# Kernel optimization log

Measured on AMD Instinct MI355X. Metric: run time of the kernel, lower is better.

## Reference

```python
import jax, jax.numpy as jnp
import numpy as np

EMBED_DIM = 32
HIDDEN_DIM = 64
N = 1024
LN_EPS = 1e-5


def setup_inputs() -> dict:
    key = jax.random.key(0)
    ks = jax.random.split(key, 8)
    d, h = EMBED_DIM, HIDDEN_DIM
    s1 = 1.0 / np.sqrt(2 * d)
    s2 = 1.0 / np.sqrt(h)
    return {
        "node_embeddings": jax.random.normal(ks[0], (N, d), dtype=jnp.float32),
        # Linear(2d -> h), stored as (2d, h) for x @ W
        "W1": jax.random.uniform(ks[1], (2 * d, h), jnp.float32, -s1, s1),
        "b1": jnp.zeros((h,), jnp.float32),
        "g1": jnp.ones((h,), jnp.float32),
        "be1": jnp.zeros((h,), jnp.float32),
        "W2": jax.random.uniform(ks[2], (h, h), jnp.float32, -s2, s2),
        "b2": jnp.zeros((h,), jnp.float32),
        "g2": jnp.ones((h,), jnp.float32),
        "be2": jnp.zeros((h,), jnp.float32),
        "W3": jax.random.uniform(ks[3], (h, 1), jnp.float32, -s2, s2),
        "b3": jnp.zeros((1,), jnp.float32),
    }


def _layernorm(x, gamma, beta):
    mu = jnp.mean(x, axis=-1, keepdims=True)
    var = jnp.mean(jnp.square(x - mu), axis=-1, keepdims=True)
    return (x - mu) * jax.lax.rsqrt(var + LN_EPS) * gamma + beta


def reference(node_embeddings, W1, b1, g1, be1, W2, b2, g2, be2, W3, b3):
    n, d = node_embeddings.shape
    # pair_emb = cat([src_emb, dst_emb], -1); first linear applied without
    # materializing the concat: split W1 into src/dst halves.
    W1s, W1d = W1[:d], W1[d:]
    hs = node_embeddings @ W1s          # (N, h)
    hd = node_embeddings @ W1d          # (N, h)
    h = hs[:, None, :] + hd[None, :, :] + b1   # (N, N, h)
    h = jax.nn.relu(_layernorm(h, g1, be1))
    h = jax.nn.relu(_layernorm(h @ W2 + b2, g2, be2))
    out = jax.nn.sigmoid((h @ W3 + b3)[..., 0])  # (N, N)
    return out
```

## Files before the change

kernel.cpp:

```cpp
#include <hip/hip_runtime.h>
#include <hip/hip_bf16.h>

#define NN 1024
#define ED 32
#define HD 64
#define LN_EPS 1e-5f
#define LPAD 68

typedef short bf16x8 __attribute__((ext_vector_type(8)));
typedef float f32x4 __attribute__((ext_vector_type(4)));

#define OFF_HS   0
#define OFF_HDB  65536
#define OFF_G1   131072
#define OFF_BE1  131136
#define OFF_B2   131200
#define OFF_G2   131264
#define OFF_BE2  131328
#define OFF_W3   131392
#define OFF_B3   131456
#define OFF_SB2  131457
#define OFF_W2F  131460

__device__ __forceinline__ bool buf_is_f32(const void* g1) {
  return *(const unsigned int*)g1 == 0x3F800000u;
}
template <bool F32>
__device__ __forceinline__ float ld(const void* p, int i) {
  return F32 ? ((const float*)p)[i]
             : __bfloat162float(((const __hip_bfloat16*)p)[i]);
}
__device__ __forceinline__ unsigned short f2bf(float f) {
  unsigned int b = __builtin_bit_cast(unsigned int, f);
  b += 0x7FFFu + ((b >> 16) & 1u);
  return (unsigned short)(b >> 16);
}
__device__ __forceinline__ unsigned int pack2bf(float a, float b) {
  return (unsigned int)f2bf(a) | ((unsigned int)f2bf(b) << 16);
}
__device__ __forceinline__ f32x4 splat4(float v) { f32x4 r = {v, v, v, v}; return r; }

template <int CTRL>
__device__ __forceinline__ float dpp_add(float v) {
  int m = __builtin_amdgcn_update_dpp(0, __builtin_bit_cast(int, v), CTRL, 0xF, 0xF, true);
  return v + __builtin_bit_cast(float, m);
}
__device__ __forceinline__ float red16(float v) {
  v = dpp_add<0xB1>(v);
  v = dpp_add<0x4E>(v);
  v = dpp_add<0x124>(v);
  v = dpp_add<0x128>(v);
  return v;
}

template <bool F32>
__device__ void prep_body(const void* E, const void* W1, const void* b1,
                          const void* g1, const void* be1, const void* W2,
                          const void* b2, const void* g2, const void* be2,
                          const void* W3, const void* b3, float* ws) {
  const int i = blockIdx.x, t = threadIdx.x;
  if (i < NN) {
    __shared__ float e[ED];
    if (t < ED) e[t] = ld<F32>(E, i * ED + t);
    __syncthreads();
    int k = t & 63;
    int wofs = (t >= 64 ? ED * HD : 0);
    float acc = 0.f;
#pragma unroll
    for (int c = 0; c < ED; ++c)
      acc = fmaf(e[c], ld<F32>(W1, wofs + c * HD + k), acc);
    if (t >= 64) ws[OFF_HDB + i * HD + k] = acc + ld<F32>(b1, k);
    else         ws[OFF_HS  + i * HD + k] = acc;
  } else {
    __shared__ float rs[64];
    if (t < 64) {
      ws[OFF_G1  + t] = ld<F32>(g1,  t);
      ws[OFF_BE1 + t] = ld<F32>(be1, t);
      ws[OFF_B2  + t] = ld<F32>(b2,  t);
      ws[OFF_G2  + t] = ld<F32>(g2,  t);
      ws[OFF_BE2 + t] = ld<F32>(be2, t);
      ws[OFF_W3  + t] = ld<F32>(W3,  t);
      float s = 0.f;
      for (int n = 0; n < HD; ++n) s += ld<F32>(W2, t * HD + n);
      rs[t] = s;
    }
    if (t == 64) {
      float s = 0.f;
      for (int n = 0; n < HD; ++n) s += ld<F32>(b2, n);
      ws[OFF_SB2] = s;
    }
    if (t == 65) ws[OFF_B3] = ld<F32>(b3, 0);
    uint4* d4 = (uint4*)(ws + OFF_W2F);
    for (int base = t * 16; base < 4096; base += 128 * 16) {
      int nt = (base >> 9) & 3, kc = base >> 11;
#pragma unroll
      for (int half = 0; half < 2; ++half) {
        int lv = ((base >> 3) + half) & 63;
        int k0 = kc * 32 + ((lv >> 4) & 3) * 8;
        int n = nt * 16 + (lv & 15);
        unsigned int u4[4];
#pragma unroll
        for (int jj = 0; jj < 4; ++jj)
          u4[jj] = pack2bf(ld<F32>(W2, (k0 + 2 * jj) * HD + n),
                           ld<F32>(W2, (k0 + 2 * jj + 1) * HD + n));
        d4[(base >> 3) + half] = make_uint4(u4[0], u4[1], u4[2], u4[3]);
      }
    }
    __syncthreads();
    unsigned short* st = (unsigned short*)(ws + OFF_W2F) + 4096;
    for (int s = t; s < 1024; s += 128) {
      int j = s & 7, lv = (s >> 3) & 63, kc = s >> 9;
      st[s] = f2bf(rs[kc * 32 + ((lv >> 4) & 3) * 8 + j]);
    }
  }
}

__global__ __launch_bounds__(128) void prep_kern(
    const void* E, const void* W1, const void* b1, const void* g1,
    const void* be1, const void* W2, const void* b2, const void* g2,
    const void* be2, const void* W3, const void* b3, float* ws) {
  if (buf_is_f32(g1))
    prep_body<true >(E, W1, b1, g1, be1, W2, b2, g2, be2, W3, b3, ws);
  else
    prep_body<false>(E, W1, b1, g1, be1, W2, b2, g2, be2, W3, b3, ws);
}

__global__ __launch_bounds__(256, 3) void pair_kern(
    const float* __restrict__ ws, float* __restrict__ out) {
  __shared__ float shsd[2][16 * LPAD];
  __shared__ __align__(16) unsigned int X[256 * 32];
  const int t = threadIdx.x;
  const int bi = blockIdx.y, bj = blockIdx.x;
  const int l = t & 63, w = t >> 6;
  const int q = l >> 4, ln = l & 15;
  const float inv = 1.f / 64.f;

  {
    int r = t >> 4, c4 = t & 15;
    ((float4*)(shsd[0] + r * LPAD))[c4] = ((const float4*)(ws + OFF_HS  + (bi * 16 + r) * HD))[c4];
    ((float4*)(shsd[1] + r * LPAD))[c4] = ((const float4*)(ws + OFF_HDB + (bj * 16 + r) * HD))[c4];
  }
  __syncthreads();

  {
    int il = t >> 4, jl = t & 15;
    const f32x4* av = (const f32x4*)(shsd[0] + il * LPAD);
    const f32x4* bv = (const f32x4*)(shsd[1] + jl * LPAD);
    f32x4 xv[16];
    f32x4 s4 = splat4(0.f), q4 = splat4(0.f);
#pragma unroll
    for (int c = 0; c < 16; ++c) {
      f32x4 x = av[c] + bv[c];
      xv[c] = x;
      s4 += x;
      q4 = __builtin_elementwise_fma(x, x, q4);
    }
    float sum = (s4[0] + s4[1]) + (s4[2] + s4[3]);
    float ssq = (q4[0] + q4[1]) + (q4[2] + q4[3]);
    float mu = sum * inv;
    float r1 = rsqrtf(fmaf(-mu, mu, ssq * inv) + LN_EPS);
    f32x4 r1v = splat4(r1), nm = splat4(-mu * r1), zero = splat4(0.f);
    unsigned int ub[32];
#pragma unroll
    for (int c = 0; c < 16; ++c) {
      f32x4 g, be;
#pragma unroll
      for (int e = 0; e < 4; ++e) {
        g[e]  = ws[OFF_G1  + c * 4 + e];
        be[e] = ws[OFF_BE1 + c * 4 + e];
      }
      f32x4 u = __builtin_elementwise_fma(xv[c], r1v, nm);
      f32x4 v = __builtin_elementwise_fma(u, g, be);
      v = __builtin_elementwise_max(v, zero);
      ub[2 * c]     = pack2bf(v[0], v[1]);
      ub[2 * c + 1] = pack2bf(v[2], v[3]);
    }
    uint4* Xr4 = (uint4*)(X + t * 32);
#pragma unroll
    for (int b = 0; b < 8; ++b)
      Xr4[b ^ (t & 7)] = make_uint4(ub[4 * b], ub[4 * b + 1], ub[4 * b + 2], ub[4 * b + 3]);
  }
  __syncthreads();

  bf16x8 bf[2][4], bsum[2];
  const uint4* WF4 = (const uint4*)(ws + OFF_W2F);
#pragma unroll
  for (int kc = 0; kc < 2; ++kc) {
#pragma unroll
    for (int nt = 0; nt < 4; ++nt)
      bf[kc][nt] = __builtin_bit_cast(bf16x8, WF4[(kc * 4 + nt) * 64 + l]);
    bsum[kc] = __builtin_bit_cast(bf16x8, WF4[512 + kc * 64 + l]);
  }
  f32x4 acc[4][5];
  const uint4* XL = (const uint4*)X;
#pragma unroll
  for (int mt = 0; mt < 4; ++mt) {
    int m = w * 64 + mt * 16 + ln;
    bf16x8 a0 = __builtin_bit_cast(bf16x8, XL[m * 8 + (q ^ (m & 7))]);
    bf16x8 a1 = __builtin_bit_cast(bf16x8, XL[m * 8 + ((q + 4) ^ (m & 7))]);
#pragma unroll
    for (int nt = 0; nt < 5; ++nt) {
      bf16x8 b0  = (nt < 4) ? bf[0][nt] : bsum[0];
      bf16x8 b1f = (nt < 4) ? bf[1][nt] : bsum[1];
      f32x4 z4 = splat4(0.f);
      z4 = __builtin_amdgcn_mfma_f32_16x16x32_bf16(a0, b0, z4, 0, 0, 0);
      acc[mt][nt] = __builtin_amdgcn_mfma_f32_16x16x32_bf16(a1, b1f, z4, 0, 0, 0);
    }
  }

  float b2v[4], g2v[4], be2v[4], w3v[4];
#pragma unroll
  for (int nt = 0; nt < 4; ++nt) {
    int cix = nt * 16 + ln;
    b2v[nt]  = ws[OFF_B2  + cix];
    g2v[nt]  = ws[OFF_G2  + cix];
    be2v[nt] = ws[OFF_BE2 + cix];
    w3v[nt]  = ws[OFF_W3  + cix];
  }
  const float b3s = ws[OFF_B3];
  const float Sb2 = ws[OFF_SB2];

#pragma unroll
  for (int mt = 0; mt < 4; ++mt) {
    f32x4 y[4], qq = splat4(0.f);
#pragma unroll
    for (int nt = 0; nt < 4; ++nt) {
      y[nt] = acc[mt][nt] + splat4(b2v[nt]);
      qq = __builtin_elementwise_fma(y[nt], y[nt], qq);
    }
#pragma unroll
    for (int e = 0; e < 4; ++e) qq[e] = red16(qq[e]);
    f32x4 s4 = acc[mt][4] + splat4(Sb2);
    f32x4 mu = s4 * inv;
    f32x4 var = qq * inv - mu * mu;
    f32x4 r2;
#pragma unroll
    for (int e = 0; e < 4; ++e) r2[e] = rsqrtf(var[e] + LN_EPS);
    f32x4 z4 = splat4(0.f);
#pragma unroll
    for (int nt = 0; nt < 4; ++nt) {
      f32x4 u = (y[nt] - mu) * r2;
      f32x4 v = __builtin_elementwise_fma(u, splat4(g2v[nt]), splat4(be2v[nt]));
      v = __builtin_elementwise_max(v, splat4(0.f));
      z4 = __builtin_elementwise_fma(v, splat4(w3v[nt]), z4);
    }
#pragma unroll
    for (int e = 0; e < 4; ++e) z4[e] = red16(z4[e]);
#pragma unroll
    for (int reg = 0; reg < 4; ++reg) {
      float z = z4[reg] + b3s;
      float o = 1.f / (1.f + __expf(-z));
      if (ln == reg) {
        int irow = bi * 16 + (w * 4 + mt);
        int jcol = bj * 16 + (q * 4 + reg);
        out[irow * NN + jcol] = o;
      }
    }
  }
}

extern "C" void kernel_launch(void* const* d_in, const int* in_sizes, int n_in,
                              void* d_out, int out_size, void* d_ws, size_t ws_size,
                              hipStream_t stream) {
  float* ws = (float*)d_ws;
  hipLaunchKernelGGL(prep_kern, dim3(NN + 1), dim3(128), 0, stream,
                     d_in[0], d_in[1], d_in[2], d_in[3], d_in[4], d_in[5],
                     d_in[6], d_in[7], d_in[8], d_in[9], d_in[10], ws);
  hipLaunchKernelGGL(pair_kern, dim3(64, 64), dim3(256), 0, stream,
                     ws, (float*)d_out);
}
```

Before: 128.7 us.

## Precompute row sums, swizzle LDS, drop barrier, spread W2 packing, raise occupancy

The prep kernel now stores per-row sums of hs and hd so the pair kernel gets the first LayerNorm mean without summing the 64 features. The padded LDS tiles become XOR-swizzled tiles. The barrier after writing X is removed, because each wave reads only rows written by its own lanes. W2 fragment packing is spread across 16 extra prep blocks. Launch bounds go from 3 to 4 blocks per CU, bf16 packing uses the intrinsic converter, and the output store picks its value with selects instead of a per-register loop. Together these aim to cut ALU work, LDS conflicts and synchronisation, at the risk of register pressure under the tighter launch bound.

```diff
diff --git a/kernel.cpp b/kernel.cpp
--- a/kernel.cpp
+++ b/kernel.cpp
@@ -5,22 +5,23 @@
 #define ED 32
 #define HD 64
 #define LN_EPS 1e-5f
-#define LPAD 68
 
 typedef short bf16x8 __attribute__((ext_vector_type(8)));
 typedef float f32x4 __attribute__((ext_vector_type(4)));
 
 #define OFF_HS   0
 #define OFF_HDB  65536
-#define OFF_G1   131072
-#define OFF_BE1  131136
-#define OFF_B2   131200
-#define OFF_G2   131264
-#define OFF_BE2  131328
-#define OFF_W3   131392
-#define OFF_B3   131456
-#define OFF_SB2  131457
-#define OFF_W2F  131460
+#define OFF_SS   131072
+#define OFF_SD   132096
+#define OFF_G1   133120
+#define OFF_BE1  133184
+#define OFF_B2   133248
+#define OFF_G2   133312
+#define OFF_BE2  133376
+#define OFF_W3   133440
+#define OFF_B3   133504
+#define OFF_SB2  133505
+#define OFF_W2F  133508
 
 __device__ __forceinline__ bool buf_is_f32(const void* g1) {
   return *(const unsigned int*)g1 == 0x3F800000u;
@@ -37,6 +38,12 @@
 }
 __device__ __forceinline__ unsigned int pack2bf(float a, float b) {
   return (unsigned int)f2bf(a) | ((unsigned int)f2bf(b) << 16);
+}
+__device__ __forceinline__ unsigned int pk_bf(float a, float b) {
+  __hip_bfloat162 p = __float22bfloat162_rn(make_float2(a, b));
+  unsigned int u;
+  __builtin_memcpy(&u, &p, 4);
+  return u;
 }
 __device__ __forceinline__ f32x4 splat4(float v) { f32x4 r = {v, v, v, v}; return r; }
 
@@ -64,13 +71,36 @@
     if (t < ED) e[t] = ld<F32>(E, i * ED + t);
     __syncthreads();
     int k = t & 63;
-    int wofs = (t >= 64 ? ED * HD : 0);
+    bool dside = t >= 64;
+    int wofs = dside ? ED * HD : 0;
     float acc = 0.f;
 #pragma unroll
     for (int c = 0; c < ED; ++c)
       acc = fmaf(e[c], ld<F32>(W1, wofs + c * HD + k), acc);
-    if (t >= 64) ws[OFF_HDB + i * HD + k] = acc + ld<F32>(b1, k);
-    else         ws[OFF_HS  + i * HD + k] = acc;
+    if (dside) acc += ld<F32>(b1, k);
+    float s = acc;
+#pragma unroll
+    for (int m = 1; m <= 32; m <<= 1) s += __shfl_xor(s, m);
+    if (dside) {
+      ws[OFF_HDB + i * HD + k] = acc;
+      if (k == 0) ws[OFF_SD + i] = s;
+    } else {
+      ws[OFF_HS + i * HD + k] = acc;
+      if (k == 0) ws[OFF_SS + i] = s;
+    }
+  } else if (i < NN + 16) {
+    if (t < 32) {
+      int d = (i - NN) * 32 + t;
+      int lv = d & 63, nt = (d >> 6) & 3, kc = d >> 8;
+      int k0 = kc * 32 + ((lv >> 4) & 3) * 8;
+      int n = nt * 16 + (lv & 15);
+      unsigned int u4[4];
+#pragma unroll
+      for (int jj = 0; jj < 4; ++jj)
+        u4[jj] = pack2bf(ld<F32>(W2, (k0 + 2 * jj) * HD + n),
+                         ld<F32>(W2, (k0 + 2 * jj + 1) * HD + n));
+      ((uint4*)(ws + OFF_W2F))[d] = make_uint4(u4[0], u4[1], u4[2], u4[3]);
+    }
   } else {
     __shared__ float rs[64];
     if (t < 64) {
@@ -90,22 +120,6 @@
       ws[OFF_SB2] = s;
     }
     if (t == 65) ws[OFF_B3] = ld<F32>(b3, 0);
-    uint4* d4 = (uint4*)(ws + OFF_W2F);
-    for (int base = t * 16; base < 4096; base += 128 * 16) {
-      int nt = (base >> 9) & 3, kc = base >> 11;
-#pragma unroll
-      for (int half = 0; half < 2; ++half) {
-        int lv = ((base >> 3) + half) & 63;
-        int k0 = kc * 32 + ((lv >> 4) & 3) * 8;
-        int n = nt * 16 + (lv & 15);
-        unsigned int u4[4];
-#pragma unroll
-        for (int jj = 0; jj < 4; ++jj)
-          u4[jj] = pack2bf(ld<F32>(W2, (k0 + 2 * jj) * HD + n),
-                           ld<F32>(W2, (k0 + 2 * jj + 1) * HD + n));
-        d4[(base >> 3) + half] = make_uint4(u4[0], u4[1], u4[2], u4[3]);
-      }
-    }
     __syncthreads();
     unsigned short* st = (unsigned short*)(ws + OFF_W2F) + 4096;
     for (int s = t; s < 1024; s += 128) {
@@ -125,9 +139,10 @@
     prep_body<false>(E, W1, b1, g1, be1, W2, b2, g2, be2, W3, b3, ws);
 }
 
-__global__ __launch_bounds__(256, 3) void pair_kern(
+__global__ __launch_bounds__(256, 4) void pair_kern(
     const float* __restrict__ ws, float* __restrict__ out) {
-  __shared__ float shsd[2][16 * LPAD];
+  __shared__ float sh[1024];
+  __shared__ float sdt[1024];
   __shared__ __align__(16) unsigned int X[256 * 32];
   const int t = threadIdx.x;
   const int bi = blockIdx.y, bj = blockIdx.x;
@@ -137,50 +152,51 @@
 
   {
     int r = t >> 4, c4 = t & 15;
-    ((float4*)(shsd[0] + r * LPAD))[c4] = ((const float4*)(ws + OFF_HS  + (bi * 16 + r) * HD))[c4];
-    ((float4*)(shsd[1] + r * LPAD))[c4] = ((const float4*)(ws + OFF_HDB + (bj * 16 + r) * HD))[c4];
-  }
+    ((f32x4*)sh )[r * 16 + (c4 ^ r)] = ((const f32x4*)(ws + OFF_HS  + (bi * 16 + r) * HD))[c4];
+    ((f32x4*)sdt)[r * 16 + (c4 ^ r)] = ((const f32x4*)(ws + OFF_HDB + (bj * 16 + r) * HD))[c4];
+  }
+  const int il = t >> 4, jl = t & 15;
+  const float ssum = ws[OFF_SS + bi * 16 + il];
+  const float dsum = ws[OFF_SD + bj * 16 + jl];
   __syncthreads();
 
   {
-    int il = t >> 4, jl = t & 15;
-    const f32x4* av = (const f32x4*)(shsd[0] + il * LPAD);
-    const f32x4* bv = (const f32x4*)(shsd[1] + jl * LPAD);
+    const f32x4* A4 = (const f32x4*)sh;
+    const f32x4* B4 = (const f32x4*)sdt;
     f32x4 xv[16];
-    f32x4 s4 = splat4(0.f), q4 = splat4(0.f);
+    f32x4 q4 = splat4(0.f);
 #pragma unroll
     for (int c = 0; c < 16; ++c) {
-      f32x4 x = av[c] + bv[c];
+      f32x4 x = A4[il * 16 + (c ^ il)] + B4[jl * 16 + (c ^ jl)];
       xv[c] = x;
-      s4 += x;
       q4 = __builtin_elementwise_fma(x, x, q4);
     }
-    float sum = (s4[0] + s4[1]) + (s4[2] + s4[3]);
     float ssq = (q4[0] + q4[1]) + (q4[2] + q4[3]);
-    float mu = sum * inv;
+    float mu = (ssum + dsum) * inv;
     float r1 = rsqrtf(fmaf(-mu, mu, ssq * inv) + LN_EPS);
     f32x4 r1v = splat4(r1), nm = splat4(-mu * r1), zero = splat4(0.f);
-    unsigned int ub[32];
-#pragma unroll
-    for (int c = 0; c < 16; ++c) {
-      f32x4 g, be;
-#pragma unroll
-      for (int e = 0; e < 4; ++e) {
-        g[e]  = ws[OFF_G1  + c * 4 + e];
-        be[e] = ws[OFF_BE1 + c * 4 + e];
+    uint4* Xr4 = (uint4*)(X + t * 32);
+#pragma unroll
+    for (int b = 0; b < 8; ++b) {
+      unsigned int uu[4];
+#pragma unroll
+      for (int h = 0; h < 2; ++h) {
+        int c = 2 * b + h;
+        f32x4 g, be;
+#pragma unroll
+        for (int e = 0; e < 4; ++e) {
+          g[e]  = ws[OFF_G1  + c * 4 + e];
+          be[e] = ws[OFF_BE1 + c * 4 + e];
+        }
+        f32x4 u = __builtin_elementwise_fma(xv[c], r1v, nm);
+        f32x4 v = __builtin_elementwise_fma(u, g, be);
+        v = __builtin_elementwise_max(v, zero);
+        uu[2 * h]     = pk_bf(v[0], v[1]);
+        uu[2 * h + 1] = pk_bf(v[2], v[3]);
       }
-      f32x4 u = __builtin_elementwise_fma(xv[c], r1v, nm);
-      f32x4 v = __builtin_elementwise_fma(u, g, be);
-      v = __builtin_elementwise_max(v, zero);
-      ub[2 * c]     = pack2bf(v[0], v[1]);
-      ub[2 * c + 1] = pack2bf(v[2], v[3]);
-    }
-    uint4* Xr4 = (uint4*)(X + t * 32);
-#pragma unroll
-    for (int b = 0; b < 8; ++b)
-      Xr4[b ^ (t & 7)] = make_uint4(ub[4 * b], ub[4 * b + 1], ub[4 * b + 2], ub[4 * b + 3]);
-  }
-  __syncthreads();
+      Xr4[b ^ (t & 7)] = make_uint4(uu[0], uu[1], uu[2], uu[3]);
+    }
+  }
 
   bf16x8 bf[2][4], bsum[2];
   const uint4* WF4 = (const uint4*)(ws + OFF_W2F);
@@ -246,16 +262,12 @@
     }
 #pragma unroll
     for (int e = 0; e < 4; ++e) z4[e] = red16(z4[e]);
-#pragma unroll
-    for (int reg = 0; reg < 4; ++reg) {
-      float z = z4[reg] + b3s;
-      float o = 1.f / (1.f + __expf(-z));
-      if (ln == reg) {
-        int irow = bi * 16 + (w * 4 + mt);
-        int jcol = bj * 16 + (q * 4 + reg);
-        out[irow * NN + jcol] = o;
-      }
-    }
+    float z01 = (ln & 1) ? z4[1] : z4[0];
+    float z23 = (ln & 1) ? z4[3] : z4[2];
+    float zs = ((ln & 2) ? z23 : z01) + b3s;
+    float o = 1.f / (1.f + __expf(-zs));
+    if (ln < 4)
+      out[(bi * 16 + w * 4 + mt) * NN + bj * 16 + q * 4 + ln] = o;
   }
 }
 
@@ -263,7 +275,7 @@
                               void* d_out, int out_size, void* d_ws, size_t ws_size,
                               hipStream_t stream) {
   float* ws = (float*)d_ws;
-  hipLaunchKernelGGL(prep_kern, dim3(NN + 1), dim3(128), 0, stream,
+  hipLaunchKernelGGL(prep_kern, dim3(NN + 17), dim3(128), 0, stream,
                      d_in[0], d_in[1], d_in[2], d_in[3], d_in[4], d_in[5],
                      d_in[6], d_in[7], d_in[8], d_in[9], d_in[10], ws);
   hipLaunchKernelGGL(pair_kern, dim3(64, 64), dim3(256), 0, stream,
```

New measurement: 119.5 us. 7.1% less time.
